# Kernel optimization log

Hardware: AMD Instinct MI355X
Metric: run time of the kernel (lower is better)

## Reference

```python
import jax, jax.numpy as jnp
import numpy as np

U = 128  # linear_units

def setup_inputs() -> dict:
    key = jax.random.key(0)
    k1, k2, k3, k4, k5, k6 = jax.random.split(key, 6)
    B, S, D = 16, 2048, 128
    x = jax.random.normal(k1, (B, S, D), dtype=jnp.float32)
    t = jax.random.uniform(k2, (B, S), dtype=jnp.float32)
    # glorot_uniform inits
    lim_qk = np.sqrt(6.0 / (D + U)).astype(np.float32)
    Wq = jax.random.uniform(k3, (D, U), minval=-lim_qk, maxval=lim_qk, dtype=jnp.float32)
    Wk = jax.random.uniform(k4, (D, U), minval=-lim_qk, maxval=lim_qk, dtype=jnp.float32)
    lim_s = np.sqrt(6.0 / (1 + S)).astype(np.float32)
    theta = jax.random.uniform(k5, (1, S), minval=-lim_s, maxval=lim_s, dtype=jnp.float32)
    mu = jax.random.uniform(k6, (1, S), minval=-lim_s, maxval=lim_s, dtype=jnp.float32)
    return {"x": x, "t": t, "Wq": Wq, "Wk": Wk, "theta": theta, "mu": mu}

def reference(x, t, Wq, Wk, theta, mu):
    # x: (B,S,D), t: (B,S), theta/mu: (1,S)
    scale = jnp.sqrt(jnp.asarray(U, dtype=x.dtype))
    q = x @ Wq                                   # (B,S,U)
    k = x @ Wk                                   # (B,S,U)
    scores = jnp.einsum('biu,bju->bij', q, k) / scale  # (B,S,S)
    alphas = jax.nn.softmax(scores, axis=-1)
    gn = jnp.einsum('bij,bjd->bid', alphas, x)   # weighted sum == alphas @ x, (B,S,D)
    time_fact = jax.nn.sigmoid(theta - mu * t)   # (B,S)
    v = jnp.sum(gn * time_fact[:, :, None], axis=1)  # (B,D)
    return v
```

## Files before the change

kernel.cpp:

```cpp
#include <hip/hip_runtime.h>
#include <hip/hip_bf16.h>

#define SS 2048
#define DD 128
#define BB 16
#define LDST 136
#define SCT 268

typedef short bf16x8 __attribute__((ext_vector_type(8)));
typedef float f32x4 __attribute__((ext_vector_type(4)));
typedef unsigned short ushort_t;

#define SB0() __builtin_amdgcn_sched_barrier(0)
#define WAITV(n) asm volatile("s_waitcnt vmcnt(" #n ")" ::: "memory")

__device__ __forceinline__ unsigned short f2bf(float f) {
  union { float f; unsigned u; } v; v.f = f;
  unsigned r = v.u + 0x7fffu + ((v.u >> 16) & 1u);
  return (unsigned short)(r >> 16);
}
__device__ __forceinline__ float fexp2(float x) { return __builtin_amdgcn_exp2f(x); }


__global__ __launch_bounds__(256) void wprep(
    const float* __restrict__ Wq, const float* __restrict__ Wk,
    ushort_t* __restrict__ wt_g) {
  int idx = blockIdx.x * 256 + threadIdx.x;
  int r = idx & 16383, uu = r >> 7, d = r & 127;
  if (idx < 16384)
    wt_g[uu * 128 + d] = f2bf(Wq[d * 128 + uu] * 0.1275174346f);
  else
    wt_g[(uu + 128) * 128 + d] = f2bf(Wk[d * 128 + uu]);
}

__global__ __launch_bounds__(256, 2) void qk_gemm(
    const float* __restrict__ x, const ushort_t* __restrict__ wt_g,
    uint4* __restrict__ qF, uint4* __restrict__ kF) {
  __shared__ ushort_t xs[64 * LDST];
  __shared__ ushort_t sc[64 * SCT];
  const int tid = threadIdx.x, wave = tid >> 6, lane = tid & 63;
  const int lq = lane & 15, quad = lane >> 4;
  const int m0 = blockIdx.x * 64;

#pragma unroll
  for (int i = 0; i < 8; ++i) {
    int idx = i * 256 + tid;
    int row = idx >> 5, c4 = (idx & 31) * 4;
    const float4 v = *(const float4*)(x + (size_t)(m0 + row) * DD + c4);
    ushort4 h;
    h.x = f2bf(v.x); h.y = f2bf(v.y); h.z = f2bf(v.z); h.w = f2bf(v.w);
    *(ushort4*)(&xs[row * LDST + c4]) = h;
  }
  bf16x8 wf[4][4];
#pragma unroll
  for (int nt = 0; nt < 4; ++nt)
#pragma unroll
    for (int ks = 0; ks < 4; ++ks)
      wf[nt][ks] = *(const bf16x8*)(wt_g + (wave * 64 + nt * 16 + lq) * 128 + ks * 32 + quad * 8);
  __syncthreads();

  f32x4 acc[4][4];
#pragma unroll
  for (int mt = 0; mt < 4; ++mt)
#pragma unroll
    for (int nt = 0; nt < 4; ++nt) acc[mt][nt] = (f32x4){0.f, 0.f, 0.f, 0.f};
#pragma unroll
  for (int mt = 0; mt < 4; ++mt) {
    bf16x8 af[4];
#pragma unroll
    for (int ks = 0; ks < 4; ++ks)
      af[ks] = *(const bf16x8*)(&xs[(mt * 16 + lq) * LDST + ks * 32 + quad * 8]);
#pragma unroll
    for (int nt = 0; nt < 4; ++nt)
#pragma unroll
      for (int ks = 0; ks < 4; ++ks)
        acc[mt][nt] = __builtin_amdgcn_mfma_f32_16x16x32_bf16(af[ks], wf[nt][ks], acc[mt][nt], 0, 0, 0);
  }
#pragma unroll
  for (int mt = 0; mt < 4; ++mt)
#pragma unroll
    for (int nt = 0; nt < 4; ++nt)
#pragma unroll
      for (int r = 0; r < 4; ++r)
        sc[(mt * 16 + quad * 4 + r) * SCT + wave * 64 + nt * 16 + lq] = f2bf(acc[mt][nt][r]);
  __syncthreads();
#pragma unroll
  for (int i = 0; i < 8; ++i) {
    int c = i * 256 + tid;
    int lane_c = c & 63, ks_c = (c >> 6) & 3, g_c = (c >> 8) & 3, isk = c >> 10;
    int li = lane_c & 15, qd = lane_c >> 4;
    int col = isk * 128 + ks_c * 32 + qd * 8;
    uint4 v = *(const uint4*)(&sc[(g_c * 16 + li) * SCT + col]);
    size_t G = (size_t)blockIdx.x * 4 + g_c;
    uint4* dst = isk ? kF : qF;
    dst[(G * 4 + ks_c) * 64 + lane_c] = v;
  }
}

__global__ __launch_bounds__(256, 2) void attn_fused(
    const uint4* __restrict__ qF, const uint4* __restrict__ kF,
    const float* __restrict__ t, const float* __restrict__ theta,
    const float* __restrict__ mu, float* __restrict__ w) {
  const int xcd = blockIdx.x & 7, s = blockIdx.x >> 3;
  const int b = xcd + ((s >> 5) << 3);
  const int ib = s & 31;
  const int i0 = ib * 64;
  const int tid = threadIdx.x, wave = tid >> 6, lane = tid & 63;
  const int lq = lane & 15, quad = lane >> 4;

  __shared__ float rs_lds[4][64];
  __shared__ float c_lds[64];

  const bf16x8* qc = (const bf16x8*)qF;

  bf16x8 af[4][4];
#pragma unroll
  for (int mt = 0; mt < 4; ++mt)
#pragma unroll
    for (int ks = 0; ks < 4; ++ks)
      af[mt][ks] = qc[((size_t)(b * 128 + ib * 4 + mt) * 4 + ks) * 64 + lane];

  const bf16x8* kb = (const bf16x8*)kF + (size_t)b * 128 * 4 * 64 + lane;
  auto loadg = [&](bf16x8 (&f)[4], int g) {
#pragma unroll
    for (int ks = 0; ks < 4; ++ks)
      f[ks] = kb[((size_t)g * 4 + ks) * 64];
  };
  auto G = [&](int m) { return (m >> 1) * 8 + wave * 2 + (m & 1); };

  const f32x4 z4 = {0.f, 0.f, 0.f, 0.f};
  auto mfma16 = [&](f32x4 (&a)[4], bf16x8 (&f)[4]) {
    __builtin_amdgcn_s_setprio(1);
#pragma unroll
    for (int mt = 0; mt < 4; ++mt)
      a[mt] = __builtin_amdgcn_mfma_f32_16x16x32_bf16(af[mt][0], f[0], z4, 0, 0, 0);
#pragma unroll
    for (int ks = 1; ks < 4; ++ks)
#pragma unroll
      for (int mt = 0; mt < 4; ++mt)
        a[mt] = __builtin_amdgcn_mfma_f32_16x16x32_bf16(af[mt][ks], f[ks], a[mt], 0, 0, 0);
    __builtin_amdgcn_s_setprio(0);
  };

  float rowsum[4][4];
#pragma unroll
  for (int mt = 0; mt < 4; ++mt)
#pragma unroll
    for (int r = 0; r < 4; ++r) rowsum[mt][r] = 0.f;
  auto proc1 = [&](f32x4 (&a)[4]) {
#pragma unroll
    for (int mt = 0; mt < 4; ++mt)
#pragma unroll
      for (int r = 0; r < 4; ++r) rowsum[mt][r] += fexp2(a[mt][r]);
  };

  bf16x8 fA[4], fB[4];
  f32x4 a[4];

  loadg(fA, G(0));
  loadg(fB, G(1));
  for (int m = 0; m < 30; m += 2) {
    WAITV(4); SB0();
    mfma16(a, fA);
    loadg(fA, G(m + 2)); SB0();
    proc1(a);
    WAITV(4); SB0();
    mfma16(a, fB);
    loadg(fB, G(m + 3)); SB0();
    proc1(a);
  }
  WAITV(4); SB0(); mfma16(a, fA); SB0(); proc1(a);
  WAITV(0); SB0(); mfma16(a, fB); SB0(); proc1(a);

#pragma unroll
  for (int d2 = 1; d2 <= 8; d2 <<= 1)
#pragma unroll
    for (int mt = 0; mt < 4; ++mt)
#pragma unroll
      for (int r = 0; r < 4; ++r)
        rowsum[mt][r] += __shfl_xor(rowsum[mt][r], d2, 64);
  if (lq == 0) {
#pragma unroll
    for (int mt = 0; mt < 4; ++mt)
#pragma unroll
      for (int r = 0; r < 4; ++r)
        rs_lds[wave][mt * 16 + quad * 4 + r] = rowsum[mt][r];
  }
  __syncthreads();
  if (tid < 64) {
    float l = rs_lds[0][tid] + rs_lds[1][tid] + rs_lds[2][tid] + rs_lds[3][tid];
    int gi = i0 + tid;
    float z = theta[gi] - mu[gi] * t[b * SS + gi];
    float tf = 1.f / (1.f + fexp2(-z * 1.44269504f));
    c_lds[tid] = tf / l;
  }
  __syncthreads();
  float creg[4][4];
#pragma unroll
  for (int mt = 0; mt < 4; ++mt)
#pragma unroll
    for (int r = 0; r < 4; ++r) creg[mt][r] = c_lds[mt * 16 + quad * 4 + r];

  auto proc2 = [&](f32x4 (&aa)[4], int g) {
    float cs = 0.f;
#pragma unroll
    for (int mt = 0; mt < 4; ++mt)
#pragma unroll
      for (int r = 0; r < 4; ++r) cs = fmaf(creg[mt][r], fexp2(aa[mt][r]), cs);
    cs += __shfl_xor(cs, 16, 64);
    cs += __shfl_xor(cs, 32, 64);
    if (lane < 16) atomicAdd(&w[b * SS + g * 16 + lane], cs);
  };

  loadg(fA, G(0));
  loadg(fB, G(1));
  for (int m = 0; m < 30; m += 2) {
    WAITV(4); SB0();
    mfma16(a, fA);
    loadg(fA, G(m + 2)); SB0();
    proc2(a, G(m));
    WAITV(4); SB0();
    mfma16(a, fB);
    loadg(fB, G(m + 3)); SB0();
    proc2(a, G(m + 1));
  }
  WAITV(4); SB0(); mfma16(a, fA); SB0(); proc2(a, G(30));
  WAITV(0); SB0(); mfma16(a, fB); SB0(); proc2(a, G(31));
}

__global__ __launch_bounds__(256) void finalize(
    const float* __restrict__ x, const float* __restrict__ w,
    float* __restrict__ out) {
  const int b = blockIdx.x >> 5;
  const int j0 = (blockIdx.x & 31) * 64;
  const int tid = threadIdx.x;
  const int d4 = (tid & 31) * 4, jo = tid >> 5;
  float4 a0 = {0.f, 0.f, 0.f, 0.f}, a1 = {0.f, 0.f, 0.f, 0.f};
#pragma unroll
  for (int jj = 0; jj < 4; ++jj) {
    int ja = j0 + jj * 16 + jo, jb = ja + 8;
    float wa = w[b * SS + ja], wb = w[b * SS + jb];
    const float4 xa = *(const float4*)(x + ((size_t)b * SS + ja) * DD + d4);
    const float4 xb = *(const float4*)(x + ((size_t)b * SS + jb) * DD + d4);
    a0.x = fmaf(wa, xa.x, a0.x); a0.y = fmaf(wa, xa.y, a0.y);
    a0.z = fmaf(wa, xa.z, a0.z); a0.w = fmaf(wa, xa.w, a0.w);
    a1.x = fmaf(wb, xb.x, a1.x); a1.y = fmaf(wb, xb.y, a1.y);
    a1.z = fmaf(wb, xb.z, a1.z); a1.w = fmaf(wb, xb.w, a1.w);
  }
  __shared__ float4 red[256];
  float4 acc = {a0.x + a1.x, a0.y + a1.y, a0.z + a1.z, a0.w + a1.w};
  red[tid] = acc;
  __syncthreads();
  if (tid < 128) {
    float4 o = red[tid + 128];
    red[tid].x += o.x; red[tid].y += o.y; red[tid].z += o.z; red[tid].w += o.w;
  }
  __syncthreads();
  if (tid < 64) {
    float4 o = red[tid + 64];
    red[tid].x += o.x; red[tid].y += o.y; red[tid].z += o.z; red[tid].w += o.w;
  }
  __syncthreads();
  if (tid < 32) {
    float4 v = red[tid], o = red[tid + 32];
    v.x += o.x; v.y += o.y; v.z += o.z; v.w += o.w;
    atomicAdd(&out[b * DD + d4 + 0], v.x);
    atomicAdd(&out[b * DD + d4 + 1], v.y);
    atomicAdd(&out[b * DD + d4 + 2], v.z);
    atomicAdd(&out[b * DD + d4 + 3], v.w);
  }
}

extern "C" void kernel_launch(void* const* d_in, const int* in_sizes, int n_in,
                              void* d_out, int out_size, void* d_ws, size_t ws_size,
                              hipStream_t stream) {
  const float* x = (const float*)d_in[0];
  const float* t = (const float*)d_in[1];
  const float* Wq = (const float*)d_in[2];
  const float* Wk = (const float*)d_in[3];
  const float* theta = (const float*)d_in[4];
  const float* mu = (const float*)d_in[5];
  float* out = (float*)d_out;

  uint4* qF = (uint4*)d_ws;
  uint4* kF = qF + (size_t)2048 * 4 * 64;
  ushort_t* wt_g = (ushort_t*)(kF + (size_t)2048 * 4 * 64);
  float* w = (float*)(wt_g + 256 * 128);

  hipMemsetAsync(w, 0, (size_t)BB * SS * sizeof(float), stream);
  hipMemsetAsync(d_out, 0, (size_t)BB * DD * sizeof(float), stream);

  wprep<<<dim3(128), dim3(256), 0, stream>>>(Wq, Wk, wt_g);
  qk_gemm<<<dim3(512), dim3(256), 0, stream>>>(x, wt_g, qF, kF);
  attn_fused<<<dim3(512), dim3(256), 0, stream>>>(qF, kF, t, theta, mu, w);
  finalize<<<dim3(512), dim3(256), 0, stream>>>(x, w, out);
}
```

Baseline: 127.2 us.

## Split attention into two kernels with per-wave query tiles and shared key ranges

Splits the fused attention kernel into two kernels. The first computes softmax row sums and accumulates them atomically into a global buffer. The second computes the time-weighted column weights. Each block now gives every wave its own 16 query rows and has all four waves walk the same 32-group key range, with periodic barriers, so key loads are shared across waves in cache instead of being spread out. The cost is an extra launch, an extra memset, atomics on the row sums, and a redundant load of the Q fragments in the second kernel.

```diff
diff --git a/kernel.cpp b/kernel.cpp
--- a/kernel.cpp
+++ b/kernel.cpp
@@ -97,36 +97,35 @@
   }
 }
 
-__global__ __launch_bounds__(256, 2) void attn_fused(
+__device__ __forceinline__ void attn_decode(int bx, int& b, int& ii, int& jq) {
+  int xcd = bx & 7, s = bx >> 3;
+  b = xcd + ((s >> 5) << 3);
+  int r = s & 31;
+  ii = r >> 2;
+  jq = r & 3;
+}
+
+__global__ __launch_bounds__(256, 2) void attn_p1(
     const uint4* __restrict__ qF, const uint4* __restrict__ kF,
-    const float* __restrict__ t, const float* __restrict__ theta,
-    const float* __restrict__ mu, float* __restrict__ w) {
-  const int xcd = blockIdx.x & 7, s = blockIdx.x >> 3;
-  const int b = xcd + ((s >> 5) << 3);
-  const int ib = s & 31;
-  const int i0 = ib * 64;
+    float* __restrict__ l) {
+  int b, ii, jq;
+  attn_decode(blockIdx.x, b, ii, jq);
   const int tid = threadIdx.x, wave = tid >> 6, lane = tid & 63;
   const int lq = lane & 15, quad = lane >> 4;
 
-  __shared__ float rs_lds[4][64];
-  __shared__ float c_lds[64];
-
   const bf16x8* qc = (const bf16x8*)qF;
-
   bf16x8 af[4][4];
 #pragma unroll
   for (int mt = 0; mt < 4; ++mt)
 #pragma unroll
     for (int ks = 0; ks < 4; ++ks)
-      af[mt][ks] = qc[((size_t)(b * 128 + ib * 4 + mt) * 4 + ks) * 64 + lane];
+      af[mt][ks] = qc[((size_t)(b * 128 + ii * 16 + wave * 4 + mt) * 4 + ks) * 64 + lane];
 
   const bf16x8* kb = (const bf16x8*)kF + (size_t)b * 128 * 4 * 64 + lane;
   auto loadg = [&](bf16x8 (&f)[4], int g) {
 #pragma unroll
-    for (int ks = 0; ks < 4; ++ks)
-      f[ks] = kb[((size_t)g * 4 + ks) * 64];
-  };
-  auto G = [&](int m) { return (m >> 1) * 8 + wave * 2 + (m & 1); };
+    for (int ks = 0; ks < 4; ++ks) f[ks] = kb[((size_t)g * 4 + ks) * 64];
+  };
 
   const f32x4 z4 = {0.f, 0.f, 0.f, 0.f};
   auto mfma16 = [&](f32x4 (&a)[4], bf16x8 (&f)[4]) {
@@ -154,19 +153,21 @@
       for (int r = 0; r < 4; ++r) rowsum[mt][r] += fexp2(a[mt][r]);
   };
 
+  const int g0 = jq * 32;
   bf16x8 fA[4], fB[4];
   f32x4 a[4];
 
-  loadg(fA, G(0));
-  loadg(fB, G(1));
+  loadg(fA, g0);
+  loadg(fB, g0 + 1);
   for (int m = 0; m < 30; m += 2) {
+    if ((m & 7) == 0) __builtin_amdgcn_s_barrier();
     WAITV(4); SB0();
     mfma16(a, fA);
-    loadg(fA, G(m + 2)); SB0();
+    loadg(fA, g0 + m + 2); SB0();
     proc1(a);
     WAITV(4); SB0();
     mfma16(a, fB);
-    loadg(fB, G(m + 3)); SB0();
+    loadg(fB, g0 + m + 3); SB0();
     proc1(a);
   }
   WAITV(4); SB0(); mfma16(a, fA); SB0(); proc1(a);
@@ -184,48 +185,94 @@
     for (int mt = 0; mt < 4; ++mt)
 #pragma unroll
       for (int r = 0; r < 4; ++r)
-        rs_lds[wave][mt * 16 + quad * 4 + r] = rowsum[mt][r];
-  }
-  __syncthreads();
-  if (tid < 64) {
-    float l = rs_lds[0][tid] + rs_lds[1][tid] + rs_lds[2][tid] + rs_lds[3][tid];
-    int gi = i0 + tid;
+        atomicAdd(&l[b * SS + (ii * 16 + wave * 4 + mt) * 16 + quad * 4 + r],
+                  rowsum[mt][r]);
+  }
+}
+
+__global__ __launch_bounds__(256, 2) void attn_p2(
+    const uint4* __restrict__ qF, const uint4* __restrict__ kF,
+    const float* __restrict__ t, const float* __restrict__ theta,
+    const float* __restrict__ mu, const float* __restrict__ l,
+    float* __restrict__ w) {
+  int b, ii, jq;
+  attn_decode(blockIdx.x, b, ii, jq);
+  const int tid = threadIdx.x, wave = tid >> 6, lane = tid & 63;
+  const int lq = lane & 15, quad = lane >> 4;
+  __shared__ float c_lds[256];
+
+  {
+    int gi = ii * 256 + tid;
     float z = theta[gi] - mu[gi] * t[b * SS + gi];
     float tf = 1.f / (1.f + fexp2(-z * 1.44269504f));
-    c_lds[tid] = tf / l;
-  }
+    c_lds[tid] = tf / l[b * SS + gi];
+  }
+
+  const bf16x8* qc = (const bf16x8*)qF;
+  bf16x8 af[4][4];
+#pragma unroll
+  for (int mt = 0; mt < 4; ++mt)
+#pragma unroll
+    for (int ks = 0; ks < 4; ++ks)
+      af[mt][ks] = qc[((size_t)(b * 128 + ii * 16 + wave * 4 + mt) * 4 + ks) * 64 + lane];
+
+  const bf16x8* kb = (const bf16x8*)kF + (size_t)b * 128 * 4 * 64 + lane;
+  auto loadg = [&](bf16x8 (&f)[4], int g) {
+#pragma unroll
+    for (int ks = 0; ks < 4; ++ks) f[ks] = kb[((size_t)g * 4 + ks) * 64];
+  };
+
   __syncthreads();
   float creg[4][4];
 #pragma unroll
   for (int mt = 0; mt < 4; ++mt)
 #pragma unroll
-    for (int r = 0; r < 4; ++r) creg[mt][r] = c_lds[mt * 16 + quad * 4 + r];
-
-  auto proc2 = [&](f32x4 (&aa)[4], int g) {
+    for (int r = 0; r < 4; ++r)
+      creg[mt][r] = c_lds[(wave * 4 + mt) * 16 + quad * 4 + r];
+
+  const f32x4 z4 = {0.f, 0.f, 0.f, 0.f};
+  auto mfma16 = [&](f32x4 (&a)[4], bf16x8 (&f)[4]) {
+    __builtin_amdgcn_s_setprio(1);
+#pragma unroll
+    for (int mt = 0; mt < 4; ++mt)
+      a[mt] = __builtin_amdgcn_mfma_f32_16x16x32_bf16(af[mt][0], f[0], z4, 0, 0, 0);
+#pragma unroll
+    for (int ks = 1; ks < 4; ++ks)
+#pragma unroll
+      for (int mt = 0; mt < 4; ++mt)
+        a[mt] = __builtin_amdgcn_mfma_f32_16x16x32_bf16(af[mt][ks], f[ks], a[mt], 0, 0, 0);
+    __builtin_amdgcn_s_setprio(0);
+  };
+  auto proc2 = [&](f32x4 (&a)[4], int g) {
     float cs = 0.f;
 #pragma unroll
     for (int mt = 0; mt < 4; ++mt)
 #pragma unroll
-      for (int r = 0; r < 4; ++r) cs = fmaf(creg[mt][r], fexp2(aa[mt][r]), cs);
+      for (int r = 0; r < 4; ++r) cs = fmaf(creg[mt][r], fexp2(a[mt][r]), cs);
     cs += __shfl_xor(cs, 16, 64);
     cs += __shfl_xor(cs, 32, 64);
     if (lane < 16) atomicAdd(&w[b * SS + g * 16 + lane], cs);
   };
 
-  loadg(fA, G(0));
-  loadg(fB, G(1));
+  const int g0 = jq * 32;
+  bf16x8 fA[4], fB[4];
+  f32x4 a[4];
+
+  loadg(fA, g0);
+  loadg(fB, g0 + 1);
   for (int m = 0; m < 30; m += 2) {
+    if ((m & 7) == 0) __builtin_amdgcn_s_barrier();
     WAITV(4); SB0();
     mfma16(a, fA);
-    loadg(fA, G(m + 2)); SB0();
-    proc2(a, G(m));
+    loadg(fA, g0 + m + 2); SB0();
+    proc2(a, g0 + m);
     WAITV(4); SB0();
     mfma16(a, fB);
-    loadg(fB, G(m + 3)); SB0();
-    proc2(a, G(m + 1));
-  }
-  WAITV(4); SB0(); mfma16(a, fA); SB0(); proc2(a, G(30));
-  WAITV(0); SB0(); mfma16(a, fB); SB0(); proc2(a, G(31));
+    loadg(fB, g0 + m + 3); SB0();
+    proc2(a, g0 + m + 1);
+  }
+  WAITV(4); SB0(); mfma16(a, fA); SB0(); proc2(a, g0 + 30);
+  WAITV(0); SB0(); mfma16(a, fB); SB0(); proc2(a, g0 + 31);
 }
 
 __global__ __launch_bounds__(256) void finalize(
@@ -286,12 +333,15 @@
   uint4* kF = qF + (size_t)2048 * 4 * 64;
   ushort_t* wt_g = (ushort_t*)(kF + (size_t)2048 * 4 * 64);
   float* w = (float*)(wt_g + 256 * 128);
+  float* l = w + (size_t)BB * SS;
 
   hipMemsetAsync(w, 0, (size_t)BB * SS * sizeof(float), stream);
+  hipMemsetAsync(l, 0, (size_t)BB * SS * sizeof(float), stream);
   hipMemsetAsync(d_out, 0, (size_t)BB * DD * sizeof(float), stream);
 
   wprep<<<dim3(128), dim3(256), 0, stream>>>(Wq, Wk, wt_g);
   qk_gemm<<<dim3(512), dim3(256), 0, stream>>>(x, wt_g, qF, kF);
-  attn_fused<<<dim3(512), dim3(256), 0, stream>>>(qF, kF, t, theta, mu, w);
+  attn_p1<<<dim3(512), dim3(256), 0, stream>>>(qF, kF, l);
+  attn_p2<<<dim3(512), dim3(256), 0, stream>>>(qF, kF, t, theta, mu, l, w);
   finalize<<<dim3(512), dim3(256), 0, stream>>>(x, w, out);
 }
```

Result: slower. 130.6 us (+2.6%).

## Software-pipeline MFMA of next tile with exp processing of previous tile

Applied to the files above, without the earlier changes.

Double-buffers the score accumulators so each step issues the MFMAs for tile m+1 while the exp/rowsum (or weighted-sum) work for tile m runs. Sched-group barriers interleave one MFMA with two VALU ops. The weighted sum in the second pass is split into four independent accumulators to shorten the dependency chain. This should hide the transcendental and VALU latency behind matrix-core work, at the cost of extra accumulator registers and more complex loop prologue and epilogue handling.

```diff
diff --git a/kernel.cpp b/kernel.cpp
--- a/kernel.cpp
+++ b/kernel.cpp
@@ -13,6 +13,10 @@
 
 #define SB0() __builtin_amdgcn_sched_barrier(0)
 #define WAITV(n) asm volatile("s_waitcnt vmcnt(" #n ")" ::: "memory")
+#define SGB_MFMA1_VALU2() \
+  do { _Pragma("unroll") for (int _k = 0; _k < 16; ++_k) { \
+    __builtin_amdgcn_sched_group_barrier(0x008, 1, 0); \
+    __builtin_amdgcn_sched_group_barrier(0x002, 2, 0); } } while (0)
 
 __device__ __forceinline__ unsigned short f2bf(float f) {
   union { float f; unsigned u; } v; v.f = f;
@@ -112,7 +116,6 @@
   __shared__ float c_lds[64];
 
   const bf16x8* qc = (const bf16x8*)qF;
-
   bf16x8 af[4][4];
 #pragma unroll
   for (int mt = 0; mt < 4; ++mt)
@@ -130,7 +133,6 @@
 
   const f32x4 z4 = {0.f, 0.f, 0.f, 0.f};
   auto mfma16 = [&](f32x4 (&a)[4], bf16x8 (&f)[4]) {
-    __builtin_amdgcn_s_setprio(1);
 #pragma unroll
     for (int mt = 0; mt < 4; ++mt)
       a[mt] = __builtin_amdgcn_mfma_f32_16x16x32_bf16(af[mt][0], f[0], z4, 0, 0, 0);
@@ -139,7 +141,6 @@
 #pragma unroll
       for (int mt = 0; mt < 4; ++mt)
         a[mt] = __builtin_amdgcn_mfma_f32_16x16x32_bf16(af[mt][ks], f[ks], a[mt], 0, 0, 0);
-    __builtin_amdgcn_s_setprio(0);
   };
 
   float rowsum[4][4];
@@ -153,24 +154,35 @@
 #pragma unroll
       for (int r = 0; r < 4; ++r) rowsum[mt][r] += fexp2(a[mt][r]);
   };
+  auto step1 = [&](f32x4 (&ad)[4], bf16x8 (&f)[4], f32x4 (&as)[4]) {
+    __builtin_amdgcn_s_setprio(1);
+    mfma16(ad, f);
+    proc1(as);
+    SGB_MFMA1_VALU2();
+    __builtin_amdgcn_s_setprio(0);
+  };
 
   bf16x8 fA[4], fB[4];
-  f32x4 a[4];
+  f32x4 aA[4], aB[4];
 
   loadg(fA, G(0));
   loadg(fB, G(1));
+  WAITV(4); SB0();
+  mfma16(aA, fA);
+  loadg(fA, G(2)); SB0();
   for (int m = 0; m < 30; m += 2) {
     WAITV(4); SB0();
-    mfma16(a, fA);
-    loadg(fA, G(m + 2)); SB0();
-    proc1(a);
+    step1(aB, fB, aA);
+    loadg(fB, G(m + 3)); SB0();
     WAITV(4); SB0();
-    mfma16(a, fB);
-    loadg(fB, G(m + 3)); SB0();
-    proc1(a);
-  }
-  WAITV(4); SB0(); mfma16(a, fA); SB0(); proc1(a);
-  WAITV(0); SB0(); mfma16(a, fB); SB0(); proc1(a);
+    step1(aA, fA, aB);
+    if (m < 28) { loadg(fA, G(m + 4)); }
+    SB0();
+  }
+  WAITV(0); SB0();
+  step1(aB, fB, aA);
+  SB0();
+  proc1(aB);
 
 #pragma unroll
   for (int d2 = 1; d2 <= 8; d2 <<= 1)
@@ -201,31 +213,46 @@
 #pragma unroll
     for (int r = 0; r < 4; ++r) creg[mt][r] = c_lds[mt * 16 + quad * 4 + r];
 
-  auto proc2 = [&](f32x4 (&aa)[4], int g) {
-    float cs = 0.f;
-#pragma unroll
-    for (int mt = 0; mt < 4; ++mt)
-#pragma unroll
-      for (int r = 0; r < 4; ++r) cs = fmaf(creg[mt][r], fexp2(aa[mt][r]), cs);
+  auto proc2 = [&](f32x4 (&a)[4], int g) {
+    float c0 = 0.f, c1 = 0.f, c2 = 0.f, c3 = 0.f;
+#pragma unroll
+    for (int mt = 0; mt < 4; ++mt) {
+      c0 = fmaf(creg[mt][0], fexp2(a[mt][0]), c0);
+      c1 = fmaf(creg[mt][1], fexp2(a[mt][1]), c1);
+      c2 = fmaf(creg[mt][2], fexp2(a[mt][2]), c2);
+      c3 = fmaf(creg[mt][3], fexp2(a[mt][3]), c3);
+    }
+    float cs = (c0 + c1) + (c2 + c3);
     cs += __shfl_xor(cs, 16, 64);
     cs += __shfl_xor(cs, 32, 64);
     if (lane < 16) atomicAdd(&w[b * SS + g * 16 + lane], cs);
   };
+  auto step2 = [&](f32x4 (&ad)[4], bf16x8 (&f)[4], f32x4 (&as)[4], int g) {
+    __builtin_amdgcn_s_setprio(1);
+    mfma16(ad, f);
+    proc2(as, g);
+    SGB_MFMA1_VALU2();
+    __builtin_amdgcn_s_setprio(0);
+  };
 
   loadg(fA, G(0));
   loadg(fB, G(1));
+  WAITV(4); SB0();
+  mfma16(aA, fA);
+  loadg(fA, G(2)); SB0();
   for (int m = 0; m < 30; m += 2) {
     WAITV(4); SB0();
-    mfma16(a, fA);
-    loadg(fA, G(m + 2)); SB0();
-    proc2(a, G(m));
+    step2(aB, fB, aA, G(m));
+    loadg(fB, G(m + 3)); SB0();
     WAITV(4); SB0();
-    mfma16(a, fB);
-    loadg(fB, G(m + 3)); SB0();
-    proc2(a, G(m + 1));
-  }
-  WAITV(4); SB0(); mfma16(a, fA); SB0(); proc2(a, G(30));
-  WAITV(0); SB0(); mfma16(a, fB); SB0(); proc2(a, G(31));
+    step2(aA, fA, aB, G(m + 1));
+    if (m < 28) { loadg(fA, G(m + 4)); }
+    SB0();
+  }
+  WAITV(0); SB0();
+  step2(aB, fB, aA, G(30));
+  SB0();
+  proc2(aB, G(31));
 }
 
 __global__ __launch_bounds__(256) void finalize(
```

After: 129.5 us. Within noise of the previous version (+1.8%).

## Split QK projection across Q/K halves and tile the weight transpose

Applied to the files above, without the earlier changes.

The qk_gemm kernel now launches twice as many blocks, each computing only the Q or the K half for a 64-row tile. This halves per-block registers and LDS so occupancy can rise to 4 blocks per CU, at the cost of each x tile being loaded and converted twice. The weight-prep kernel becomes an LDS-tiled transpose with coalesced reads and writes instead of strided gathers. A scheduling barrier also splits the x loads into two batches.

```diff
diff --git a/kernel.cpp b/kernel.cpp
--- a/kernel.cpp
+++ b/kernel.cpp
@@ -5,7 +5,7 @@
 #define DD 128
 #define BB 16
 #define LDST 136
-#define SCT 268
+#define SCT2 134
 
 typedef short bf16x8 __attribute__((ext_vector_type(8)));
 typedef float f32x4 __attribute__((ext_vector_type(4)));
@@ -25,25 +25,44 @@
 __global__ __launch_bounds__(256) void wprep(
     const float* __restrict__ Wq, const float* __restrict__ Wk,
     ushort_t* __restrict__ wt_g) {
-  int idx = blockIdx.x * 256 + threadIdx.x;
-  int r = idx & 16383, uu = r >> 7, d = r & 127;
-  if (idx < 16384)
-    wt_g[uu * 128 + d] = f2bf(Wq[d * 128 + uu] * 0.1275174346f);
-  else
-    wt_g[(uu + 128) * 128 + d] = f2bf(Wk[d * 128 + uu]);
-}
-
-__global__ __launch_bounds__(256, 2) void qk_gemm(
+  const int isK = blockIdx.x >> 2, ut = (blockIdx.x >> 1) & 1, dt = blockIdx.x & 1;
+  const int tid = threadIdx.x;
+  const float* W = isK ? Wk : Wq;
+  const float scale = isK ? 1.0f : 0.1275174346f;
+  __shared__ float tile[64][65];
+
+  {
+    int uu = tid & 63, dr = tid >> 6;
+#pragma unroll
+    for (int p = 0; p < 16; ++p) {
+      int d = p * 4 + dr;
+      tile[uu][d] = W[(size_t)(dt * 64 + d) * 128 + ut * 64 + uu];
+    }
+  }
+  __syncthreads();
+  {
+    int d = tid & 63, ur = tid >> 6;
+#pragma unroll
+    for (int p = 0; p < 16; ++p) {
+      int uu = p * 4 + ur;
+      wt_g[(size_t)(isK * 128 + ut * 64 + uu) * 128 + dt * 64 + d] =
+          f2bf(tile[uu][d] * scale);
+    }
+  }
+}
+
+__global__ __launch_bounds__(256, 4) void qk_gemm(
     const float* __restrict__ x, const ushort_t* __restrict__ wt_g,
     uint4* __restrict__ qF, uint4* __restrict__ kF) {
   __shared__ ushort_t xs[64 * LDST];
-  __shared__ ushort_t sc[64 * SCT];
+  __shared__ ushort_t sc[64 * SCT2];
   const int tid = threadIdx.x, wave = tid >> 6, lane = tid & 63;
   const int lq = lane & 15, quad = lane >> 4;
-  const int m0 = blockIdx.x * 64;
-
-#pragma unroll
-  for (int i = 0; i < 8; ++i) {
+  const int rb = blockIdx.x >> 1, ch = blockIdx.x & 1;
+  const int m0 = rb * 64;
+
+#pragma unroll
+  for (int i = 0; i < 4; ++i) {
     int idx = i * 256 + tid;
     int row = idx >> 5, c4 = (idx & 31) * 4;
     const float4 v = *(const float4*)(x + (size_t)(m0 + row) * DD + c4);
@@ -51,19 +70,30 @@
     h.x = f2bf(v.x); h.y = f2bf(v.y); h.z = f2bf(v.z); h.w = f2bf(v.w);
     *(ushort4*)(&xs[row * LDST + c4]) = h;
   }
-  bf16x8 wf[4][4];
-#pragma unroll
-  for (int nt = 0; nt < 4; ++nt)
+  SB0();
+#pragma unroll
+  for (int i = 4; i < 8; ++i) {
+    int idx = i * 256 + tid;
+    int row = idx >> 5, c4 = (idx & 31) * 4;
+    const float4 v = *(const float4*)(x + (size_t)(m0 + row) * DD + c4);
+    ushort4 h;
+    h.x = f2bf(v.x); h.y = f2bf(v.y); h.z = f2bf(v.z); h.w = f2bf(v.w);
+    *(ushort4*)(&xs[row * LDST + c4]) = h;
+  }
+  bf16x8 wf[2][4];
+#pragma unroll
+  for (int nt = 0; nt < 2; ++nt)
 #pragma unroll
     for (int ks = 0; ks < 4; ++ks)
-      wf[nt][ks] = *(const bf16x8*)(wt_g + (wave * 64 + nt * 16 + lq) * 128 + ks * 32 + quad * 8);
-  __syncthreads();
-
-  f32x4 acc[4][4];
-#pragma unroll
-  for (int mt = 0; mt < 4; ++mt)
-#pragma unroll
-    for (int nt = 0; nt < 4; ++nt) acc[mt][nt] = (f32x4){0.f, 0.f, 0.f, 0.f};
+      wf[nt][ks] = *(const bf16x8*)(wt_g +
+          (size_t)(ch * 128 + wave * 32 + nt * 16 + lq) * 128 + ks * 32 + quad * 8);
+  __syncthreads();
+
+  f32x4 acc[4][2];
+#pragma unroll
+  for (int mt = 0; mt < 4; ++mt)
+#pragma unroll
+    for (int nt = 0; nt < 2; ++nt) acc[mt][nt] = (f32x4){0.f, 0.f, 0.f, 0.f};
 #pragma unroll
   for (int mt = 0; mt < 4; ++mt) {
     bf16x8 af[4];
@@ -71,7 +101,7 @@
     for (int ks = 0; ks < 4; ++ks)
       af[ks] = *(const bf16x8*)(&xs[(mt * 16 + lq) * LDST + ks * 32 + quad * 8]);
 #pragma unroll
-    for (int nt = 0; nt < 4; ++nt)
+    for (int nt = 0; nt < 2; ++nt)
 #pragma unroll
       for (int ks = 0; ks < 4; ++ks)
         acc[mt][nt] = __builtin_amdgcn_mfma_f32_16x16x32_bf16(af[ks], wf[nt][ks], acc[mt][nt], 0, 0, 0);
@@ -79,20 +109,20 @@
 #pragma unroll
   for (int mt = 0; mt < 4; ++mt)
 #pragma unroll
-    for (int nt = 0; nt < 4; ++nt)
+    for (int nt = 0; nt < 2; ++nt)
 #pragma unroll
       for (int r = 0; r < 4; ++r)
-        sc[(mt * 16 + quad * 4 + r) * SCT + wave * 64 + nt * 16 + lq] = f2bf(acc[mt][nt][r]);
-  __syncthreads();
-#pragma unroll
-  for (int i = 0; i < 8; ++i) {
+        sc[(mt * 16 + quad * 4 + r) * SCT2 + wave * 32 + nt * 16 + lq] = f2bf(acc[mt][nt][r]);
+  __syncthreads();
+#pragma unroll
+  for (int i = 0; i < 4; ++i) {
     int c = i * 256 + tid;
-    int lane_c = c & 63, ks_c = (c >> 6) & 3, g_c = (c >> 8) & 3, isk = c >> 10;
+    int lane_c = c & 63, ks_c = (c >> 6) & 3, g_c = (c >> 8) & 3;
     int li = lane_c & 15, qd = lane_c >> 4;
-    int col = isk * 128 + ks_c * 32 + qd * 8;
-    uint4 v = *(const uint4*)(&sc[(g_c * 16 + li) * SCT + col]);
-    size_t G = (size_t)blockIdx.x * 4 + g_c;
-    uint4* dst = isk ? kF : qF;
+    int col = ks_c * 32 + qd * 8;
+    uint4 v = *(const uint4*)(&sc[(g_c * 16 + li) * SCT2 + col]);
+    size_t G = (size_t)rb * 4 + g_c;
+    uint4* dst = ch ? kF : qF;
     dst[(G * 4 + ks_c) * 64 + lane_c] = v;
   }
 }
@@ -112,7 +142,6 @@
   __shared__ float c_lds[64];
 
   const bf16x8* qc = (const bf16x8*)qF;
-
   bf16x8 af[4][4];
 #pragma unroll
   for (int mt = 0; mt < 4; ++mt)
@@ -290,8 +319,8 @@
   hipMemsetAsync(w, 0, (size_t)BB * SS * sizeof(float), stream);
   hipMemsetAsync(d_out, 0, (size_t)BB * DD * sizeof(float), stream);
 
-  wprep<<<dim3(128), dim3(256), 0, stream>>>(Wq, Wk, wt_g);
-  qk_gemm<<<dim3(512), dim3(256), 0, stream>>>(x, wt_g, qF, kF);
+  wprep<<<dim3(8), dim3(256), 0, stream>>>(Wq, Wk, wt_g);
+  qk_gemm<<<dim3(1024), dim3(256), 0, stream>>>(x, wt_g, qF, kF);
   attn_fused<<<dim3(512), dim3(256), 0, stream>>>(qF, kF, t, theta, mu, w);
   finalize<<<dim3(512), dim3(256), 0, stream>>>(x, w, out);
 }
```

New measurement: 127.5 us. About the same (+0.2%).
